# Kernel optimization log

Measured on AMD Instinct MI355X. Metric: run time of the kernel, lower is better.

Reference implementation:

```python
import jax, jax.numpy as jnp
import numpy as np
from jax import lax

WIN = 5
WIN_SIZE = float(WIN * WIN * WIN)


def _box_sum(x):
    # 5x5x5 all-ones box-filter sum, stride 1, padding 2 (SAME), single channel.
    k = jnp.ones((1, 1, WIN, WIN, WIN), dtype=x.dtype)
    return lax.conv_general_dilated(
        x, k,
        window_strides=(1, 1, 1),
        padding=[(2, 2), (2, 2), (2, 2)],
        dimension_numbers=('NCDHW', 'OIDHW', 'NCDHW'))


def setup_inputs() -> dict:
    key = jax.random.key(0)
    k1, k2 = jax.random.split(key)
    shape = (2, 1, 160, 160, 160)
    real = jax.random.normal(k1, shape, dtype=jnp.float32)
    fake = jax.random.normal(k2, shape, dtype=jnp.float32)
    return {"real": real, "fake": fake}


def reference(real, fake):
    I2 = real * real
    J2 = fake * fake
    IJ = real * fake
    I_sum = _box_sum(real)
    J_sum = _box_sum(fake)
    I2_sum = _box_sum(I2)
    J2_sum = _box_sum(J2)
    IJ_sum = _box_sum(IJ)
    u_I = I_sum / WIN_SIZE
    u_J = J_sum / WIN_SIZE
    cross = IJ_sum - u_J * I_sum - u_I * J_sum + u_I * u_J * WIN_SIZE
    I_var = I2_sum - 2.0 * u_I * I_sum + u_I * u_I * WIN_SIZE
    J_var = J2_sum - 2.0 * u_J * J_sum + u_J * u_J * WIN_SIZE
    cc = cross * cross / (I_var * J_var + 1e-05)
    return jnp.mean(cc)
```

## Files before the change

### kernel.cpp

```cpp
#include <hip/hip_runtime.h>


#define DIM 160
#define SLAB (DIM * DIM)
#define VOL (DIM * DIM * DIM)
#define TD 8
#define TH 16
#define ROWS 20
#define RST 44
#define NBLK 2000
#define NPART (NBLK * 4)

typedef float f4 __attribute__((ext_vector_type(4), aligned(16)));
typedef float f2 __attribute__((ext_vector_type(2), aligned(8)));

__global__ __launch_bounds__(256, 2) void ncc_main(const float* __restrict__ real,
                                                   const float* __restrict__ fake,
                                                   float* __restrict__ partials) {
    __shared__ __align__(16) float raw[2][2][ROWS][RST];

    const int tid = threadIdx.x;

    const int bid = blockIdx.x;
    const int vid = (bid & 7) * 250 + (bid >> 3);
    const int dz  = vid % 20;
    const int t1  = vid / 20;
    const int bx  = t1 % 5;
    const int by  = (t1 / 5) % 10;
    const int nb  = t1 / 50;
    const int w0 = 32 * bx, h0 = TH * by, d0 = TD * dz;

    const float* baseI = real + (size_t)nb * VOL;
    const float* baseJ = fake + (size_t)nb * VOL;

    const int sc = tid & 15;
    const int sr = tid >> 4;
    const int co = sr * RST + 2 * sc + 2;

    int gof[2], lof[2];
    bool ok[2];
    const float* src[2];
#pragma unroll
    for (int k = 0; k < 2; ++k) {
        const int t   = tid + 256 * k;
        const int vv  = t / 200;
        const int rem = t - 200 * vv;
        const int row = rem / 10;
        const int q   = rem - 10 * row;
        const int hg  = h0 - 2 + row;
        const int wq  = w0 - 4 + 4 * q;
        ok[k]  = (t < 400) && ((unsigned)hg < DIM) && (wq >= 0) && (wq + 3 < DIM);
        gof[k] = hg * DIM + wq;
        lof[k] = (vv * ROWS + row) * RST + 4 * q;
        src[k] = vv ? baseJ : baseI;
    }

    {
        float* L = &raw[0][0][0][0];
        for (int i = tid; i < 880; i += 256) *(f4*)(L + 4 * i) = (f4){0.f, 0.f, 0.f, 0.f};
    }
    __syncthreads();

    if (d0 > 0) {
        const size_t so = (size_t)(d0 - 2) * SLAB;
        float* L = &raw[0][0][0][0];
#pragma unroll
        for (int k = 0; k < 2; ++k)
            if (ok[k]) *(f4*)(L + lof[k]) = *(const f4*)(src[k] + so + gof[k]);
    }
    __syncthreads();

    const f2 z2 = (f2){0.f, 0.f};
    const f4 zf = (f4){0.f, 0.f, 0.f, 0.f};
    f2 zs[5][5];
#pragma unroll
    for (int p = 0; p < 5; ++p)
#pragma unroll
        for (int q = 0; q < 5; ++q) zs[p][q] = z2;

    f2 acc = z2;
    const float inv = 1.0f / 125.0f;
    int cur = 0;

#pragma unroll 1
    for (int a = 0; a < 3; ++a) {
        const bool am0 = (a > 0);
#pragma unroll
        for (int b = 0; b < 5; ++b) {
            const bool compAct  = (a < 2) || (b < 2);
            const bool stageAct = (a < 2) || (b == 0);
            if (!compAct) continue;

            f4 v0 = zf, v1 = zf;
            if (stageAct) {
                const int dd1 = d0 - 1 + 5 * a + b;
                if ((unsigned)dd1 < DIM) {
                    const size_t so = (size_t)dd1 * SLAB;
                    if (ok[0]) v0 = *(const f4*)(src[0] + so + gof[0]);
                    if (ok[1]) v1 = *(const f4*)(src[1] + so + gof[1]);
                }
            }

            const float* LB = &raw[cur][0][0][0];
            f2 A0 = z2, A1 = z2, A2v = z2, B0 = z2, B1 = z2, B2v = z2;
            f2 A20 = z2, A21 = z2, A22 = z2, B20 = z2, B21 = z2, B22 = z2;
            f2 P0 = z2, P1 = z2, P2 = z2;
#pragma unroll
            for (int t = 0; t < 5; ++t) {
                const float* rp = LB + co + t * RST;
                const f2 a0 = *(const f2*)(rp);
                const f2 a1 = *(const f2*)(rp + 2);
                const f2 a2 = *(const f2*)(rp + 4);
                const f2 b0 = *(const f2*)(rp + ROWS * RST);
                const f2 b1 = *(const f2*)(rp + ROWS * RST + 2);
                const f2 b2 = *(const f2*)(rp + ROWS * RST + 4);
                A0 += a0; A1 += a1; A2v += a2;
                B0 += b0; B1 += b1; B2v += b2;
                A20 += a0 * a0; A21 += a1 * a1; A22 += a2 * a2;
                B20 += b0 * b0; B21 += b1 * b1; B22 += b2 * b2;
                P0 += a0 * b0; P1 += a1 * b1; P2 += a2 * b2;
            }
#define HW2(r0, r1, r2) ((f2){((r0.x + r0.y) + (r1.x + r1.y)) + r2.x, \
                              ((r0.y + r1.x) + (r1.y + r2.x)) + r2.y})
            const f2 cs0 = HW2(A0, A1, A2v);
            const f2 cs1 = HW2(B0, B1, B2v);
            const f2 cs2 = HW2(A20, A21, A22);
            const f2 cs3 = HW2(B20, B21, B22);
            const f2 cs4 = HW2(P0, P1, P2);
#undef HW2

#pragma unroll
            for (int p = 0; p < 5; ++p) {
                const int kk  = (b - p + 5) % 5;
                const int bmk = b - kk;
                const bool doadd = (am0 || p <= b) &&
                                   (a == 0 || (a == 1 ? (bmk <= 2) : (bmk <= -3)));
                if (doadd) {
                    zs[p][0] += cs0; zs[p][1] += cs1; zs[p][2] += cs2;
                    zs[p][3] += cs3; zs[p][4] += cs4;
                }
            }

            const bool docomp = (a == 0) ? (b == 4) : ((a == 1) ? true : (b < 2));
            if (docomp) {
                const int pe = (b + 1) % 5;
                const f2 SI = zs[pe][0], SJ = zs[pe][1];
                const f2 S2I = zs[pe][2], S2J = zs[pe][3], SIJ = zs[pe][4];
                const f2 t0    = SI * inv;
                const f2 cross = SIJ - t0 * SJ;
                const f2 iv    = S2I - t0 * SI;
                const f2 jv    = S2J - (SJ * inv) * SJ;
                acc += cross * cross / (iv * jv + 1e-5f);
                zs[pe][0] = z2; zs[pe][1] = z2; zs[pe][2] = z2;
                zs[pe][3] = z2; zs[pe][4] = z2;
            }

            if (stageAct) {
                float* LW = &raw[cur ^ 1][0][0][0];
                if (ok[0]) *(f4*)(LW + lof[0]) = v0;
                if (ok[1]) *(f4*)(LW + lof[1]) = v1;
            }
            __syncthreads();
            cur ^= 1;
        }
    }

    float a2 = acc.x + acc.y;
#pragma unroll
    for (int off = 32; off; off >>= 1)
        a2 += __shfl_down(a2, off, 64);
    if ((tid & 63) == 0)
        partials[bid * 4 + (tid >> 6)] = a2;
}

__global__ void ncc_reduce(const float* __restrict__ partials, float* __restrict__ out) {
    __shared__ double ws[4];
    double s = 0.0;
    for (int i = threadIdx.x; i < NPART; i += 256) s += (double)partials[i];
#pragma unroll
    for (int off = 32; off; off >>= 1)
        s += __shfl_down(s, off, 64);
    if ((threadIdx.x & 63) == 0) ws[threadIdx.x >> 6] = s;
    __syncthreads();
    if (threadIdx.x == 0) {
        const double t = ws[0] + ws[1] + ws[2] + ws[3];
        out[0] = (float)(t / (2.0 * (double)VOL));
    }
}

extern "C" void kernel_launch(void* const* d_in, const int* in_sizes, int n_in,
                              void* d_out, int out_size, void* d_ws, size_t ws_size,
                              hipStream_t stream) {
    const float* real = (const float*)d_in[0];
    const float* fake = (const float*)d_in[1];
    float* out      = (float*)d_out;
    float* partials = (float*)d_ws;

    ncc_main<<<dim3(NBLK), dim3(256), 0, stream>>>(real, fake, partials);
    ncc_reduce<<<1, 256, 0, stream>>>(partials, out);
}
```

Baseline: 58.15 us.

## Compute two output rows per thread with 32-row tiles to share vertical sums

```diff
diff --git a/kernel.cpp b/kernel.cpp
--- a/kernel.cpp
+++ b/kernel.cpp
@@ -5,14 +5,19 @@
 #define SLAB (DIM * DIM)
 #define VOL (DIM * DIM * DIM)
 #define TD 8
-#define TH 16
-#define ROWS 20
+#define ROWS 36
 #define RST 44
-#define NBLK 2000
+#define VOFF (ROWS * RST)
+#define NBLK 1000
 #define NPART (NBLK * 4)
 
 typedef float f4 __attribute__((ext_vector_type(4), aligned(16)));
 typedef float f2 __attribute__((ext_vector_type(2), aligned(8)));
+
+__device__ __forceinline__ f2 hw2(const f2 r0, const f2 r1, const f2 r2) {
+    const float c = (r0.y + r1.x) + r1.y;
+    return (f2){(r0.x + c) + r2.x, (c + r2.x) + r2.y};
+}
 
 __global__ __launch_bounds__(256, 2) void ncc_main(const float* __restrict__ real,
                                                    const float* __restrict__ fake,
@@ -22,42 +27,43 @@
     const int tid = threadIdx.x;
 
     const int bid = blockIdx.x;
-    const int vid = (bid & 7) * 250 + (bid >> 3);
+    const int vid = (bid & 7) * 125 + (bid >> 3);
     const int dz  = vid % 20;
     const int t1  = vid / 20;
     const int bx  = t1 % 5;
-    const int by  = (t1 / 5) % 10;
-    const int nb  = t1 / 50;
-    const int w0 = 32 * bx, h0 = TH * by, d0 = TD * dz;
+    const int by  = (t1 / 5) % 5;
+    const int nb  = t1 / 25;
+    const int w0 = 32 * bx, h0 = 32 * by, d0 = TD * dz;
 
     const float* baseI = real + (size_t)nb * VOL;
     const float* baseJ = fake + (size_t)nb * VOL;
 
     const int sc = tid & 15;
     const int sr = tid >> 4;
-    const int co = sr * RST + 2 * sc + 2;
-
-    int gof[2], lof[2];
-    bool ok[2];
-    const float* src[2];
-#pragma unroll
-    for (int k = 0; k < 2; ++k) {
+    const int co = (2 * sr) * RST + 2 * sc + 2;
+
+    int gof[3], lof[3];
+    bool ok[3];
+    const float* src[3];
+#pragma unroll
+    for (int k = 0; k < 3; ++k) {
         const int t   = tid + 256 * k;
-        const int vv  = t / 200;
-        const int rem = t - 200 * vv;
+        const int tv  = t / 360;
+        const int rem = t - 360 * tv;
         const int row = rem / 10;
         const int q   = rem - 10 * row;
         const int hg  = h0 - 2 + row;
         const int wq  = w0 - 4 + 4 * q;
-        ok[k]  = (t < 400) && ((unsigned)hg < DIM) && (wq >= 0) && (wq + 3 < DIM);
+        ok[k]  = (t < 720) && ((unsigned)hg < DIM) && (wq >= 0) && (wq + 3 < DIM);
         gof[k] = hg * DIM + wq;
-        lof[k] = (vv * ROWS + row) * RST + 4 * q;
-        src[k] = vv ? baseJ : baseI;
+        lof[k] = (tv * ROWS + row) * RST + 4 * q;
+        src[k] = tv ? baseJ : baseI;
     }
 
     {
         float* L = &raw[0][0][0][0];
-        for (int i = tid; i < 880; i += 256) *(f4*)(L + 4 * i) = (f4){0.f, 0.f, 0.f, 0.f};
+        for (int i = tid; i < 2 * 2 * ROWS * RST / 4; i += 256)
+            *(f4*)(L + 4 * i) = (f4){0.f, 0.f, 0.f, 0.f};
     }
     __syncthreads();
 
@@ -65,18 +71,18 @@
         const size_t so = (size_t)(d0 - 2) * SLAB;
         float* L = &raw[0][0][0][0];
 #pragma unroll
-        for (int k = 0; k < 2; ++k)
+        for (int k = 0; k < 3; ++k)
             if (ok[k]) *(f4*)(L + lof[k]) = *(const f4*)(src[k] + so + gof[k]);
     }
     __syncthreads();
 
     const f2 z2 = (f2){0.f, 0.f};
     const f4 zf = (f4){0.f, 0.f, 0.f, 0.f};
-    f2 zs[5][5];
+    f2 zr0[5][5], zr1[5][5];
 #pragma unroll
     for (int p = 0; p < 5; ++p)
 #pragma unroll
-        for (int q = 0; q < 5; ++q) zs[p][q] = z2;
+        for (int q = 0; q < 5; ++q) { zr0[p][q] = z2; zr1[p][q] = z2; }
 
     f2 acc = z2;
     const float inv = 1.0f / 125.0f;
@@ -91,43 +97,37 @@
             const bool stageAct = (a < 2) || (b == 0);
             if (!compAct) continue;
 
-            f4 v0 = zf, v1 = zf;
+            f4 v0 = zf, v1 = zf, v2 = zf;
             if (stageAct) {
                 const int dd1 = d0 - 1 + 5 * a + b;
                 if ((unsigned)dd1 < DIM) {
                     const size_t so = (size_t)dd1 * SLAB;
                     if (ok[0]) v0 = *(const f4*)(src[0] + so + gof[0]);
                     if (ok[1]) v1 = *(const f4*)(src[1] + so + gof[1]);
+                    if (ok[2]) v2 = *(const f4*)(src[2] + so + gof[2]);
                 }
             }
 
             const float* LB = &raw[cur][0][0][0];
-            f2 A0 = z2, A1 = z2, A2v = z2, B0 = z2, B1 = z2, B2v = z2;
-            f2 A20 = z2, A21 = z2, A22 = z2, B20 = z2, B21 = z2, B22 = z2;
-            f2 P0 = z2, P1 = z2, P2 = z2;
-#pragma unroll
-            for (int t = 0; t < 5; ++t) {
+            f2 c00 = z2, c01 = z2, c02 = z2, c03 = z2, c04 = z2;
+            f2 c10 = z2, c11 = z2, c12 = z2, c13 = z2, c14 = z2;
+#pragma unroll
+            for (int t = 0; t < 6; ++t) {
                 const float* rp = LB + co + t * RST;
                 const f2 a0 = *(const f2*)(rp);
                 const f2 a1 = *(const f2*)(rp + 2);
                 const f2 a2 = *(const f2*)(rp + 4);
-                const f2 b0 = *(const f2*)(rp + ROWS * RST);
-                const f2 b1 = *(const f2*)(rp + ROWS * RST + 2);
-                const f2 b2 = *(const f2*)(rp + ROWS * RST + 4);
-                A0 += a0; A1 += a1; A2v += a2;
-                B0 += b0; B1 += b1; B2v += b2;
-                A20 += a0 * a0; A21 += a1 * a1; A22 += a2 * a2;
-                B20 += b0 * b0; B21 += b1 * b1; B22 += b2 * b2;
-                P0 += a0 * b0; P1 += a1 * b1; P2 += a2 * b2;
-            }
-#define HW2(r0, r1, r2) ((f2){((r0.x + r0.y) + (r1.x + r1.y)) + r2.x, \
-                              ((r0.y + r1.x) + (r1.y + r2.x)) + r2.y})
-            const f2 cs0 = HW2(A0, A1, A2v);
-            const f2 cs1 = HW2(B0, B1, B2v);
-            const f2 cs2 = HW2(A20, A21, A22);
-            const f2 cs3 = HW2(B20, B21, B22);
-            const f2 cs4 = HW2(P0, P1, P2);
-#undef HW2
+                const f2 b0 = *(const f2*)(rp + VOFF);
+                const f2 b1 = *(const f2*)(rp + VOFF + 2);
+                const f2 b2 = *(const f2*)(rp + VOFF + 4);
+                const f2 w0v = hw2(a0, a1, a2);
+                const f2 w1v = hw2(b0, b1, b2);
+                const f2 w2v = hw2(a0 * a0, a1 * a1, a2 * a2);
+                const f2 w3v = hw2(b0 * b0, b1 * b1, b2 * b2);
+                const f2 w4v = hw2(a0 * b0, a1 * b1, a2 * b2);
+                if (t < 5) { c00 += w0v; c01 += w1v; c02 += w2v; c03 += w3v; c04 += w4v; }
+                if (t > 0) { c10 += w0v; c11 += w1v; c12 += w2v; c13 += w3v; c14 += w4v; }
+            }
 
 #pragma unroll
             for (int p = 0; p < 5; ++p) {
@@ -136,29 +136,45 @@
                 const bool doadd = (am0 || p <= b) &&
                                    (a == 0 || (a == 1 ? (bmk <= 2) : (bmk <= -3)));
                 if (doadd) {
-                    zs[p][0] += cs0; zs[p][1] += cs1; zs[p][2] += cs2;
-                    zs[p][3] += cs3; zs[p][4] += cs4;
+                    zr0[p][0] += c00; zr0[p][1] += c01; zr0[p][2] += c02;
+                    zr0[p][3] += c03; zr0[p][4] += c04;
+                    zr1[p][0] += c10; zr1[p][1] += c11; zr1[p][2] += c12;
+                    zr1[p][3] += c13; zr1[p][4] += c14;
                 }
             }
 
             const bool docomp = (a == 0) ? (b == 4) : ((a == 1) ? true : (b < 2));
             if (docomp) {
                 const int pe = (b + 1) % 5;
-                const f2 SI = zs[pe][0], SJ = zs[pe][1];
-                const f2 S2I = zs[pe][2], S2J = zs[pe][3], SIJ = zs[pe][4];
-                const f2 t0    = SI * inv;
-                const f2 cross = SIJ - t0 * SJ;
-                const f2 iv    = S2I - t0 * SI;
-                const f2 jv    = S2J - (SJ * inv) * SJ;
-                acc += cross * cross / (iv * jv + 1e-5f);
-                zs[pe][0] = z2; zs[pe][1] = z2; zs[pe][2] = z2;
-                zs[pe][3] = z2; zs[pe][4] = z2;
+                {
+                    const f2 SI = zr0[pe][0], SJ = zr0[pe][1];
+                    const f2 S2I = zr0[pe][2], S2J = zr0[pe][3], SIJ = zr0[pe][4];
+                    const f2 t0    = SI * inv;
+                    const f2 cross = SIJ - t0 * SJ;
+                    const f2 iv    = S2I - t0 * SI;
+                    const f2 jv    = S2J - (SJ * inv) * SJ;
+                    acc += cross * cross / (iv * jv + 1e-5f);
+                    zr0[pe][0] = z2; zr0[pe][1] = z2; zr0[pe][2] = z2;
+                    zr0[pe][3] = z2; zr0[pe][4] = z2;
+                }
+                {
+                    const f2 SI = zr1[pe][0], SJ = zr1[pe][1];
+                    const f2 S2I = zr1[pe][2], S2J = zr1[pe][3], SIJ = zr1[pe][4];
+                    const f2 t0    = SI * inv;
+                    const f2 cross = SIJ - t0 * SJ;
+                    const f2 iv    = S2I - t0 * SI;
+                    const f2 jv    = S2J - (SJ * inv) * SJ;
+                    acc += cross * cross / (iv * jv + 1e-5f);
+                    zr1[pe][0] = z2; zr1[pe][1] = z2; zr1[pe][2] = z2;
+                    zr1[pe][3] = z2; zr1[pe][4] = z2;
+                }
             }
 
             if (stageAct) {
                 float* LW = &raw[cur ^ 1][0][0][0];
                 if (ok[0]) *(f4*)(LW + lof[0]) = v0;
                 if (ok[1]) *(f4*)(LW + lof[1]) = v1;
+                if (ok[2]) *(f4*)(LW + lof[2]) = v2;
             }
             __syncthreads();
             cur ^= 1;
```

Result: faster. 55.91 us (-3.9%).

## Replace LDS staging with per-lane register columns and DPP row window sums

Applied to the files above, without the earlier changes.

```diff
diff --git a/kernel.cpp b/kernel.cpp
--- a/kernel.cpp
+++ b/kernel.cpp
@@ -5,82 +5,80 @@
 #define SLAB (DIM * DIM)
 #define VOL (DIM * DIM * DIM)
 #define TD 8
-#define TH 16
-#define ROWS 20
-#define RST 44
-#define NBLK 2000
+#define NBLK 2400
 #define NPART (NBLK * 4)
 
-typedef float f4 __attribute__((ext_vector_type(4), aligned(16)));
-typedef float f2 __attribute__((ext_vector_type(2), aligned(8)));
-
-__global__ __launch_bounds__(256, 2) void ncc_main(const float* __restrict__ real,
-                                                   const float* __restrict__ fake,
-                                                   float* __restrict__ partials) {
-    __shared__ __align__(16) float raw[2][2][ROWS][RST];
-
-    const int tid = threadIdx.x;
+template <int CTRL>
+__device__ __forceinline__ float dppf(float x) {
+    return __int_as_float(
+        __builtin_amdgcn_update_dpp(0, __float_as_int(x), CTRL, 0xF, 0xF, true));
+}
+
+__device__ __forceinline__ float win5(float v) {
+    const float p1 = dppf<0x138>(v);
+    const float p2 = dppf<0x138>(p1);
+    const float m1 = dppf<0x130>(v);
+    const float m2 = dppf<0x130>(m1);
+    return ((v + p1) + (p2 + m1)) + m2;
+}
+
+__global__ __launch_bounds__(256, 2)
+void ncc_main(const float* __restrict__ real,
+              const float* __restrict__ fake,
+              float* __restrict__ partials) {
+    const int tid  = threadIdx.x;
+    const int lane = tid & 63;
+    const int wid  = tid >> 6;
 
     const int bid = blockIdx.x;
-    const int vid = (bid & 7) * 250 + (bid >> 3);
+    const int vid = (bid & 7) * 300 + (bid >> 3);
     const int dz  = vid % 20;
-    const int t1  = vid / 20;
-    const int bx  = t1 % 5;
-    const int by  = (t1 / 5) % 10;
-    const int nb  = t1 / 50;
-    const int w0 = 32 * bx, h0 = TH * by, d0 = TD * dz;
-
-    const float* baseI = real + (size_t)nb * VOL;
-    const float* baseJ = fake + (size_t)nb * VOL;
-
-    const int sc = tid & 15;
-    const int sr = tid >> 4;
-    const int co = sr * RST + 2 * sc + 2;
-
-    int gof[2], lof[2];
-    bool ok[2];
-    const float* src[2];
-#pragma unroll
-    for (int k = 0; k < 2; ++k) {
-        const int t   = tid + 256 * k;
-        const int vv  = t / 200;
-        const int rem = t - 200 * vv;
-        const int row = rem / 10;
-        const int q   = rem - 10 * row;
-        const int hg  = h0 - 2 + row;
-        const int wq  = w0 - 4 + 4 * q;
-        ok[k]  = (t < 400) && ((unsigned)hg < DIM) && (wq >= 0) && (wq + 3 < DIM);
-        gof[k] = hg * DIM + wq;
-        lof[k] = (vv * ROWS + row) * RST + 4 * q;
-        src[k] = vv ? baseJ : baseI;
-    }
-
+    const int hb  = (vid / 20) % 20;
+    const int wt  = (vid / 400) % 3;
+    const int nb  = vid / 1200;
+    const int d0  = TD * dz;
+    const int h0  = 2 * (hb * 4 + wid);
+    const int c   = 60 * wt - 2 + lane;
+
+    const float* bI = real + (size_t)nb * VOL;
+    const float* bJ = fake + (size_t)nb * VOL;
+
+    const int   ccl = min(max(c, 0), DIM - 1);
+    const float wmf = ((unsigned)c < DIM) ? 1.f : 0.f;
+    const float om  = (lane >= 2 && lane < 62 && c < DIM) ? 1.f : 0.f;
+
+    int roff[6]; float mk[6];
+#pragma unroll
+    for (int r = 0; r < 6; ++r) {
+        const int hr = h0 - 2 + r;
+        mk[r]   = ((unsigned)hr < DIM) ? wmf : 0.f;
+        roff[r] = min(max(hr, 0), DIM - 1) * DIM + ccl;
+    }
+
+    float aI[6], aJ[6];
     {
-        float* L = &raw[0][0][0][0];
-        for (int i = tid; i < 880; i += 256) *(f4*)(L + 4 * i) = (f4){0.f, 0.f, 0.f, 0.f};
-    }
-    __syncthreads();
-
-    if (d0 > 0) {
-        const size_t so = (size_t)(d0 - 2) * SLAB;
-        float* L = &raw[0][0][0][0];
-#pragma unroll
-        for (int k = 0; k < 2; ++k)
-            if (ok[k]) *(f4*)(L + lof[k]) = *(const f4*)(src[k] + so + gof[k]);
-    }
-    __syncthreads();
-
-    const f2 z2 = (f2){0.f, 0.f};
-    const f4 zf = (f4){0.f, 0.f, 0.f, 0.f};
-    f2 zs[5][5];
+        const int dd = d0 - 2;
+        if ((unsigned)dd < DIM) {
+            const int sb = dd * SLAB;
+#pragma unroll
+            for (int r = 0; r < 6; ++r) {
+                aI[r] = bI[sb + roff[r]] * mk[r];
+                aJ[r] = bJ[sb + roff[r]] * mk[r];
+            }
+        } else {
+#pragma unroll
+            for (int r = 0; r < 6; ++r) { aI[r] = 0.f; aJ[r] = 0.f; }
+        }
+    }
+
+    float zs0[5][5], zs1[5][5];
 #pragma unroll
     for (int p = 0; p < 5; ++p)
 #pragma unroll
-        for (int q = 0; q < 5; ++q) zs[p][q] = z2;
-
-    f2 acc = z2;
+        for (int q = 0; q < 5; ++q) { zs0[p][q] = 0.f; zs1[p][q] = 0.f; }
+
+    float acc = 0.f;
     const float inv = 1.0f / 125.0f;
-    int cur = 0;
 
 #pragma unroll 1
     for (int a = 0; a < 3; ++a) {
@@ -91,43 +89,44 @@
             const bool stageAct = (a < 2) || (b == 0);
             if (!compAct) continue;
 
-            f4 v0 = zf, v1 = zf;
+            float s0[5], s1[5];
+            {
+                float q0v[5], q5v[5];
+                q0v[0] = aI[0]; q0v[1] = aJ[0];
+                q0v[2] = aI[0] * aI[0]; q0v[3] = aJ[0] * aJ[0]; q0v[4] = aI[0] * aJ[0];
+                q5v[0] = aI[5]; q5v[1] = aJ[5];
+                q5v[2] = aI[5] * aI[5]; q5v[3] = aJ[5] * aJ[5]; q5v[4] = aI[5] * aJ[5];
+#pragma unroll
+                for (int q = 0; q < 5; ++q) s0[q] = q0v[q];
+#pragma unroll
+                for (int r = 1; r < 5; ++r) {
+                    s0[0] += aI[r]; s0[1] += aJ[r];
+                    s0[2] += aI[r] * aI[r];
+                    s0[3] += aJ[r] * aJ[r];
+                    s0[4] += aI[r] * aJ[r];
+                }
+#pragma unroll
+                for (int q = 0; q < 5; ++q) s1[q] = s0[q] - q0v[q] + q5v[q];
+            }
+
             if (stageAct) {
                 const int dd1 = d0 - 1 + 5 * a + b;
                 if ((unsigned)dd1 < DIM) {
-                    const size_t so = (size_t)dd1 * SLAB;
-                    if (ok[0]) v0 = *(const f4*)(src[0] + so + gof[0]);
-                    if (ok[1]) v1 = *(const f4*)(src[1] + so + gof[1]);
-                }
-            }
-
-            const float* LB = &raw[cur][0][0][0];
-            f2 A0 = z2, A1 = z2, A2v = z2, B0 = z2, B1 = z2, B2v = z2;
-            f2 A20 = z2, A21 = z2, A22 = z2, B20 = z2, B21 = z2, B22 = z2;
-            f2 P0 = z2, P1 = z2, P2 = z2;
-#pragma unroll
-            for (int t = 0; t < 5; ++t) {
-                const float* rp = LB + co + t * RST;
-                const f2 a0 = *(const f2*)(rp);
-                const f2 a1 = *(const f2*)(rp + 2);
-                const f2 a2 = *(const f2*)(rp + 4);
-                const f2 b0 = *(const f2*)(rp + ROWS * RST);
-                const f2 b1 = *(const f2*)(rp + ROWS * RST + 2);
-                const f2 b2 = *(const f2*)(rp + ROWS * RST + 4);
-                A0 += a0; A1 += a1; A2v += a2;
-                B0 += b0; B1 += b1; B2v += b2;
-                A20 += a0 * a0; A21 += a1 * a1; A22 += a2 * a2;
-                B20 += b0 * b0; B21 += b1 * b1; B22 += b2 * b2;
-                P0 += a0 * b0; P1 += a1 * b1; P2 += a2 * b2;
-            }
-#define HW2(r0, r1, r2) ((f2){((r0.x + r0.y) + (r1.x + r1.y)) + r2.x, \
-                              ((r0.y + r1.x) + (r1.y + r2.x)) + r2.y})
-            const f2 cs0 = HW2(A0, A1, A2v);
-            const f2 cs1 = HW2(B0, B1, B2v);
-            const f2 cs2 = HW2(A20, A21, A22);
-            const f2 cs3 = HW2(B20, B21, B22);
-            const f2 cs4 = HW2(P0, P1, P2);
-#undef HW2
+                    const int sb = dd1 * SLAB;
+#pragma unroll
+                    for (int r = 0; r < 6; ++r) {
+                        aI[r] = bI[sb + roff[r]] * mk[r];
+                        aJ[r] = bJ[sb + roff[r]] * mk[r];
+                    }
+                } else {
+#pragma unroll
+                    for (int r = 0; r < 6; ++r) { aI[r] = 0.f; aJ[r] = 0.f; }
+                }
+            }
+
+            float c0[5], c1[5];
+#pragma unroll
+            for (int q = 0; q < 5; ++q) { c0[q] = win5(s0[q]); c1[q] = win5(s1[q]); }
 
 #pragma unroll
             for (int p = 0; p < 5; ++p) {
@@ -136,41 +135,45 @@
                 const bool doadd = (am0 || p <= b) &&
                                    (a == 0 || (a == 1 ? (bmk <= 2) : (bmk <= -3)));
                 if (doadd) {
-                    zs[p][0] += cs0; zs[p][1] += cs1; zs[p][2] += cs2;
-                    zs[p][3] += cs3; zs[p][4] += cs4;
+#pragma unroll
+                    for (int q = 0; q < 5; ++q) { zs0[p][q] += c0[q]; zs1[p][q] += c1[q]; }
                 }
             }
 
             const bool docomp = (a == 0) ? (b == 4) : ((a == 1) ? true : (b < 2));
             if (docomp) {
                 const int pe = (b + 1) % 5;
-                const f2 SI = zs[pe][0], SJ = zs[pe][1];
-                const f2 S2I = zs[pe][2], S2J = zs[pe][3], SIJ = zs[pe][4];
-                const f2 t0    = SI * inv;
-                const f2 cross = SIJ - t0 * SJ;
-                const f2 iv    = S2I - t0 * SI;
-                const f2 jv    = S2J - (SJ * inv) * SJ;
-                acc += cross * cross / (iv * jv + 1e-5f);
-                zs[pe][0] = z2; zs[pe][1] = z2; zs[pe][2] = z2;
-                zs[pe][3] = z2; zs[pe][4] = z2;
-            }
-
-            if (stageAct) {
-                float* LW = &raw[cur ^ 1][0][0][0];
-                if (ok[0]) *(f4*)(LW + lof[0]) = v0;
-                if (ok[1]) *(f4*)(LW + lof[1]) = v1;
-            }
-            __syncthreads();
-            cur ^= 1;
+                float cc2 = 0.f;
+                {
+                    const float SI = zs0[pe][0], SJ = zs0[pe][1];
+                    const float S2I = zs0[pe][2], S2J = zs0[pe][3], SIJ = zs0[pe][4];
+                    const float t0 = SI * inv;
+                    const float cr = SIJ - t0 * SJ;
+                    const float iv = S2I - t0 * SI;
+                    const float jv = S2J - (SJ * inv) * SJ;
+                    cc2 += cr * cr / (iv * jv + 1e-5f);
+                }
+                {
+                    const float SI = zs1[pe][0], SJ = zs1[pe][1];
+                    const float S2I = zs1[pe][2], S2J = zs1[pe][3], SIJ = zs1[pe][4];
+                    const float t0 = SI * inv;
+                    const float cr = SIJ - t0 * SJ;
+                    const float iv = S2I - t0 * SI;
+                    const float jv = S2J - (SJ * inv) * SJ;
+                    cc2 += cr * cr / (iv * jv + 1e-5f);
+                }
+                acc += om * cc2;
+#pragma unroll
+                for (int q = 0; q < 5; ++q) { zs0[pe][q] = 0.f; zs1[pe][q] = 0.f; }
+            }
         }
     }
 
-    float a2 = acc.x + acc.y;
 #pragma unroll
     for (int off = 32; off; off >>= 1)
-        a2 += __shfl_down(a2, off, 64);
-    if ((tid & 63) == 0)
-        partials[bid * 4 + (tid >> 6)] = a2;
+        acc += __shfl_down(acc, off, 64);
+    if (lane == 0)
+        partials[bid * 4 + wid] = acc;
 }
 
 __global__ void ncc_reduce(const float* __restrict__ partials, float* __restrict__ out) {
```

Result: slower. 66.98 us (+15.2%).
